# Kernel tuning notes

Hardware: AMD Instinct MI355X
Metric: run time of the kernel (lower is better)

Reference implementation:

```python
import jax, jax.numpy as jnp
import numpy as np

B, D, H = 4096, 1024, 1024  # batch, input_size, hidden_size


def setup_inputs() -> dict:
    key = jax.random.key(0)
    ks = jax.random.split(key, 7)
    stdv = 1.0 / np.sqrt(H)
    u = lambda k, shape: jax.random.uniform(k, shape, jnp.float32, -stdv, stdv)
    return {
        "x": jax.random.normal(ks[0], (B, D), jnp.float32),
        "h0": jax.random.normal(ks[1], (1, B, H), jnp.float32),
        "c0": jax.random.normal(ks[2], (1, B, H), jnp.float32),
        "w_ih": u(ks[3], (4 * H, D)),
        "w_hh": u(ks[4], (4 * H, H)),
        "b_ih": u(ks[5], (4 * H,)),
        "b_hh": u(ks[6], (4 * H,)),
    }


def lstm_cell(x, h, c, w_ih, w_hh, b_ih, b_hh):
    # gates: [B, 4H] = x @ w_ih^T + b_ih + h @ w_hh^T + b_hh
    gates = x @ w_ih.T + h @ w_hh.T + (b_ih + b_hh)
    i, f, g, o = jnp.split(gates, 4, axis=1)
    c_new = jax.nn.sigmoid(f) * c + jax.nn.sigmoid(i) * jnp.tanh(g)
    h_new = jax.nn.sigmoid(o) * jnp.tanh(c_new)
    return h_new, c_new


def reference(x, h0, c0, w_ih, w_hh, b_ih, b_hh):
    # num_layers = 1 (the only well-formed config of the original module)
    h, c = lstm_cell(x, h0[0], c0[0], w_ih, w_hh, b_ih, b_hh)
    return h, c
```

## Files before the change

kernel.cpp:

```cpp
#include <hip/hip_runtime.h>
#include <hip/hip_bf16.h>

#define TB 4096
#define TD 1024
#define TH 1024
#define TK 2048
#define KSTEPS 32

typedef _Float16 f16;
typedef _Float16 f16x8 __attribute__((ext_vector_type(8)));
typedef _Float16 f16x4 __attribute__((ext_vector_type(4)));
typedef float f32x4 __attribute__((ext_vector_type(4)));

__device__ __forceinline__ void gload16(const void* g, void* l) {
  __builtin_amdgcn_global_load_lds(
      (const __attribute__((address_space(1))) void*)g,
      (__attribute__((address_space(3))) void*)l, 16, 0, 0);
}

__global__ void __launch_bounds__(256) k_convert(
    const float* __restrict__ x, const float* __restrict__ h0,
    const float* __restrict__ w_ih, const float* __restrict__ w_hh,
    f16* __restrict__ Uh, f16* __restrict__ Wh) {
  int t = blockIdx.x * 256 + threadIdx.x;
  const int perMat = (TB * TK) / 4;
  const bool isW = t >= perMat;
  int tt = isW ? t - perMat : t;
  size_t e0 = (size_t)tt * 4;
  int row = (int)(e0 >> 11);
  int k = (int)(e0 & (TK - 1));
  const float* src;
  if (!isW)
    src = (k < TD) ? (x + (size_t)row * TD + k) : (h0 + (size_t)row * TH + (k - TD));
  else
    src = (k < TD) ? (w_ih + (size_t)row * TD + k) : (w_hh + (size_t)row * TH + (k - TD));
  float4 v = *(const float4*)src;
  f16x4 o;
  o[0] = (f16)v.x; o[1] = (f16)v.y; o[2] = (f16)v.z; o[3] = (f16)v.w;
  *(f16x4*)((isW ? Wh : Uh) + e0) = o;
}

__global__ void __launch_bounds__(256) k_lstm(
    const f16* __restrict__ Uh, const f16* __restrict__ Wh,
    const float* __restrict__ b_ih, const float* __restrict__ b_hh,
    const float* __restrict__ c0, float* __restrict__ h_out,
    float* __restrict__ c_out) {
  __shared__ char lds[32768];
  const int tid = threadIdx.x;
  const int l = tid & 63;
  const int w = tid >> 6;

  int bid = blockIdx.x;
  int swz = (bid & 7) * 128 + (bid >> 3);
  const int bm = swz >> 5;
  const int bn = swz & 31;
  const int rowBase = bm * 128;
  const int hcBase = bn * 32;

  const int srow = l >> 3;
  const int g = (l & 7) ^ srow;
  size_t aoff[4], boff[4];
#pragma unroll
  for (int j = 0; j < 4; ++j) {
    int rt = w * 32 + j * 8 + srow;
    aoff[j] = (size_t)(rowBase + rt) * TK + g * 8;
    int wr = ((rt >> 5) << 10) + hcBase + (rt & 31);
    boff[j] = (size_t)wr * TK + g * 8;
  }

  const int fr = l & 15;
  const int fq = l >> 4;
  const int s0 = ((fq ^ (fr & 7)) << 4);
  const int s1 = (((4 + fq) ^ (fr & 7)) << 4);
  const int aRow = (w * 32 + fr) * 128;

  f32x4 acc[2][8] = {};

  for (int kt = 0; kt < KSTEPS; ++kt) {
    const size_t k0 = (size_t)kt * 64;
#pragma unroll
    for (int j = 0; j < 4; ++j)
      gload16(Uh + aoff[j] + k0, lds + w * 4096 + j * 1024);
#pragma unroll
    for (int j = 0; j < 4; ++j)
      gload16(Wh + boff[j] + k0, lds + 16384 + w * 4096 + j * 1024);
    __syncthreads();

    f16x8 a[2][2];
#pragma unroll
    for (int m = 0; m < 2; ++m) {
      a[m][0] = *(const f16x8*)(lds + aRow + m * 2048 + s0);
      a[m][1] = *(const f16x8*)(lds + aRow + m * 2048 + s1);
    }
#pragma unroll
    for (int n = 0; n < 8; ++n) {
      const int bRow = 16384 + (n * 16 + fr) * 128;
      f16x8 b0 = *(const f16x8*)(lds + bRow + s0);
      f16x8 b1 = *(const f16x8*)(lds + bRow + s1);
      acc[0][n] = __builtin_amdgcn_mfma_f32_16x16x32_f16(a[0][0], b0, acc[0][n], 0, 0, 0);
      acc[1][n] = __builtin_amdgcn_mfma_f32_16x16x32_f16(a[1][0], b0, acc[1][n], 0, 0, 0);
      acc[0][n] = __builtin_amdgcn_mfma_f32_16x16x32_f16(a[0][1], b1, acc[0][n], 0, 0, 0);
      acc[1][n] = __builtin_amdgcn_mfma_f32_16x16x32_f16(a[1][1], b1, acc[1][n], 0, 0, 0);
    }
    __syncthreads();
  }

  const int cl = l & 15;
  const int rsub = fq * 4;
#pragma unroll
  for (int n0 = 0; n0 < 2; ++n0) {
    const int hc = hcBase + n0 * 16 + cl;
    const float bi = b_ih[hc] + b_hh[hc];
    const float bfv = b_ih[TH + hc] + b_hh[TH + hc];
    const float bg = b_ih[2 * TH + hc] + b_hh[2 * TH + hc];
    const float bo = b_ih[3 * TH + hc] + b_hh[3 * TH + hc];
#pragma unroll
    for (int m = 0; m < 2; ++m) {
#pragma unroll
      for (int r = 0; r < 4; ++r) {
        const int row = rowBase + w * 32 + m * 16 + rsub + r;
        float gi = acc[m][n0 + 0][r] + bi;
        float gf = acc[m][n0 + 2][r] + bfv;
        float gg = acc[m][n0 + 4][r] + bg;
        float go = acc[m][n0 + 6][r] + bo;
        float cprev = c0[(size_t)row * TH + hc];
        float ig = 1.0f / (1.0f + __expf(-gi));
        float fg = 1.0f / (1.0f + __expf(-gf));
        float og = 1.0f / (1.0f + __expf(-go));
        float cn = fg * cprev + ig * tanhf(gg);
        float hn = og * tanhf(cn);
        h_out[(size_t)row * TH + hc] = hn;
        c_out[(size_t)row * TH + hc] = cn;
      }
    }
  }
}

extern "C" void kernel_launch(void* const* d_in, const int* in_sizes, int n_in,
                              void* d_out, int out_size, void* d_ws, size_t ws_size,
                              hipStream_t stream) {
  const float* x    = (const float*)d_in[0];
  const float* h0   = (const float*)d_in[1];
  const float* c0   = (const float*)d_in[2];
  const float* w_ih = (const float*)d_in[3];
  const float* w_hh = (const float*)d_in[4];
  const float* b_ih = (const float*)d_in[5];
  const float* b_hh = (const float*)d_in[6];

  float* h_out = (float*)d_out;
  float* c_out = h_out + (size_t)TB * TH;

  f16* Uh = (f16*)d_ws;
  f16* Wh = Uh + (size_t)TB * TK;

  const int convBlocks = (2 * TB * TK / 4) / 256;
  k_convert<<<convBlocks, 256, 0, stream>>>(x, h0, w_ih, w_hh, Uh, Wh);
  k_lstm<<<1024, 256, 0, stream>>>(Uh, Wh, b_ih, b_hh, c0, h_out, c_out);
}
```

Baseline: 239.9 us.

## Enlarge GEMM tile to 256x256 with triple-buffered LDS pipeline

Moves the fused LSTM GEMM to 512-thread blocks with 256 rows by 64 hidden columns (256 gate columns), each wave computing a 128x64 sub-tile. It adds a three-stage LDS ring buffer with K-step 32, prefetches two steps ahead, and uses one barrier per step with explicit vmcnt waits, so global-to-LDS loads overlap MFMA work. The aim is more data reuse per LDS byte and hidden load latency. The cost is 96KB of dynamic LDS, more accumulator registers, and only 256 blocks for the GPU's CUs.

```diff
diff --git a/kernel.cpp b/kernel.cpp
--- a/kernel.cpp
+++ b/kernel.cpp
@@ -5,14 +5,16 @@
 #define TD 1024
 #define TH 1024
 #define TK 2048
-#define KSTEPS 32
+#define NT 64
+#define BUF_SZ 32768
+#define B_OFF 16384
 
 typedef _Float16 f16;
 typedef _Float16 f16x8 __attribute__((ext_vector_type(8)));
 typedef _Float16 f16x4 __attribute__((ext_vector_type(4)));
 typedef float f32x4 __attribute__((ext_vector_type(4)));
 
-__device__ __forceinline__ void gload16(const void* g, void* l) {
+__device__ __forceinline__ void gload16(const f16* g, const char* l) {
   __builtin_amdgcn_global_load_lds(
       (const __attribute__((address_space(1))) void*)g,
       (__attribute__((address_space(3))) void*)l, 16, 0, 0);
@@ -40,98 +42,110 @@
   *(f16x4*)((isW ? Wh : Uh) + e0) = o;
 }
 
-__global__ void __launch_bounds__(256) k_lstm(
+__global__ void __launch_bounds__(512, 2) k_lstm(
     const f16* __restrict__ Uh, const f16* __restrict__ Wh,
     const float* __restrict__ b_ih, const float* __restrict__ b_hh,
     const float* __restrict__ c0, float* __restrict__ h_out,
     float* __restrict__ c_out) {
-  __shared__ char lds[32768];
+  extern __shared__ char lds[];
   const int tid = threadIdx.x;
   const int l = tid & 63;
   const int w = tid >> 6;
+  const int wm = w >> 2;
+  const int wc = w & 3;
 
   int bid = blockIdx.x;
-  int swz = (bid & 7) * 128 + (bid >> 3);
-  const int bm = swz >> 5;
-  const int bn = swz & 31;
-  const int rowBase = bm * 128;
-  const int hcBase = bn * 32;
+  int swz = (bid & 7) * 32 + (bid >> 3);
+  const int bm = swz >> 4;
+  const int bn = swz & 15;
+  const int rowBase = bm * 256;
+  const int hcBase = bn * 64;
 
-  const int srow = l >> 3;
-  const int g = (l & 7) ^ srow;
-  size_t aoff[4], boff[4];
-#pragma unroll
-  for (int j = 0; j < 4; ++j) {
-    int rt = w * 32 + j * 8 + srow;
-    aoff[j] = (size_t)(rowBase + rt) * TK + g * 8;
-    int wr = ((rt >> 5) << 10) + hcBase + (rt & 31);
-    boff[j] = (size_t)wr * TK + g * 8;
-  }
+  const int g = (l & 3) ^ ((l >> 3) & 3);
+  const int rl = l >> 2;
+  const int cA0 = w, cA1 = 8 + w;
+  const f16* aP0 = Uh + (size_t)(rowBase + cA0 * 16 + rl) * TK + g * 8;
+  const f16* aP1 = Uh + (size_t)(rowBase + cA1 * 16 + rl) * TK + g * 8;
+  const f16* bP0 = Wh + (size_t)((cA0 & 3) * 1024 + hcBase + rl + (cA0 >> 2) * 16) * TK + g * 8;
+  const f16* bP1 = Wh + (size_t)((cA1 & 3) * 1024 + hcBase + rl + (cA1 >> 2) * 16) * TK + g * 8;
 
   const int fr = l & 15;
   const int fq = l >> 4;
-  const int s0 = ((fq ^ (fr & 7)) << 4);
-  const int s1 = (((4 + fq) ^ (fr & 7)) << 4);
-  const int aRow = (w * 32 + fr) * 128;
+  const int slot = ((fq ^ ((fr >> 1) & 3)) << 4);
+  const int aAddr = (wm * 128 + fr) * 64 + slot;
+  const int bAddr = B_OFF + (wc * 64 + fr) * 64 + slot;
 
-  f32x4 acc[2][8] = {};
+  f32x4 acc[8][4] = {};
 
-  for (int kt = 0; kt < KSTEPS; ++kt) {
-    const size_t k0 = (size_t)kt * 64;
+  gload16(aP0, lds + 0 * BUF_SZ + cA0 * 1024);
+  gload16(aP1, lds + 0 * BUF_SZ + cA1 * 1024);
+  gload16(bP0, lds + 0 * BUF_SZ + B_OFF + cA0 * 1024);
+  gload16(bP1, lds + 0 * BUF_SZ + B_OFF + cA1 * 1024);
+  gload16(aP0 + 32, lds + 1 * BUF_SZ + cA0 * 1024);
+  gload16(aP1 + 32, lds + 1 * BUF_SZ + cA1 * 1024);
+  gload16(bP0 + 32, lds + 1 * BUF_SZ + B_OFF + cA0 * 1024);
+  gload16(bP1 + 32, lds + 1 * BUF_SZ + B_OFF + cA1 * 1024);
+  asm volatile("s_waitcnt vmcnt(4)" ::: "memory");
+  __builtin_amdgcn_sched_barrier(0);
+  __builtin_amdgcn_s_barrier();
+
+  int offR = 0;
+  int offS = 2 * BUF_SZ;
+  for (int t = 0; t < NT; ++t) {
+    if (t < NT - 2) {
+      const int ke = (t + 2) * 32;
+      gload16(aP0 + ke, lds + offS + cA0 * 1024);
+      gload16(aP1 + ke, lds + offS + cA1 * 1024);
+      gload16(bP0 + ke, lds + offS + B_OFF + cA0 * 1024);
+      gload16(bP1 + ke, lds + offS + B_OFF + cA1 * 1024);
+    }
+    const char* baseA = lds + offR + aAddr;
+    const char* baseB = lds + offR + bAddr;
+    f16x8 af[8], bf[4];
 #pragma unroll
-    for (int j = 0; j < 4; ++j)
-      gload16(Uh + aoff[j] + k0, lds + w * 4096 + j * 1024);
+    for (int m = 0; m < 8; ++m) af[m] = *(const f16x8*)(baseA + m * 1024);
 #pragma unroll
-    for (int j = 0; j < 4; ++j)
-      gload16(Wh + boff[j] + k0, lds + 16384 + w * 4096 + j * 1024);
-    __syncthreads();
-
-    f16x8 a[2][2];
+    for (int n = 0; n < 4; ++n) bf[n] = *(const f16x8*)(baseB + n * 1024);
+    __builtin_amdgcn_s_setprio(1);
 #pragma unroll
-    for (int m = 0; m < 2; ++m) {
-      a[m][0] = *(const f16x8*)(lds + aRow + m * 2048 + s0);
-      a[m][1] = *(const f16x8*)(lds + aRow + m * 2048 + s1);
-    }
+    for (int m = 0; m < 8; ++m)
 #pragma unroll
-    for (int n = 0; n < 8; ++n) {
-      const int bRow = 16384 + (n * 16 + fr) * 128;
-      f16x8 b0 = *(const f16x8*)(lds + bRow + s0);
-      f16x8 b1 = *(const f16x8*)(lds + bRow + s1);
-      acc[0][n] = __builtin_amdgcn_mfma_f32_16x16x32_f16(a[0][0], b0, acc[0][n], 0, 0, 0);
-      acc[1][n] = __builtin_amdgcn_mfma_f32_16x16x32_f16(a[1][0], b0, acc[1][n], 0, 0, 0);
-      acc[0][n] = __builtin_amdgcn_mfma_f32_16x16x32_f16(a[0][1], b1, acc[0][n], 0, 0, 0);
-      acc[1][n] = __builtin_amdgcn_mfma_f32_16x16x32_f16(a[1][1], b1, acc[1][n], 0, 0, 0);
-    }
-    __syncthreads();
+      for (int n = 0; n < 4; ++n)
+        acc[m][n] = __builtin_amdgcn_mfma_f32_16x16x32_f16(af[m], bf[n], acc[m][n], 0, 0, 0);
+    __builtin_amdgcn_s_setprio(0);
+    asm volatile("s_waitcnt lgkmcnt(0)" ::: "memory");
+    if (t < NT - 2)
+      asm volatile("s_waitcnt vmcnt(4)" ::: "memory");
+    else
+      asm volatile("s_waitcnt vmcnt(0)" ::: "memory");
+    __builtin_amdgcn_sched_barrier(0);
+    __builtin_amdgcn_s_barrier();
+    offR = (offR == 2 * BUF_SZ) ? 0 : offR + BUF_SZ;
+    offS = (offS == 2 * BUF_SZ) ? 0 : offS + BUF_SZ;
   }
 
-  const int cl = l & 15;
-  const int rsub = fq * 4;
+  const int hc = hcBase + wc * 16 + fr;
+  const float bi = b_ih[hc] + b_hh[hc];
+  const float bfv = b_ih[TH + hc] + b_hh[TH + hc];
+  const float bg = b_ih[2 * TH + hc] + b_hh[2 * TH + hc];
+  const float bo = b_ih[3 * TH + hc] + b_hh[3 * TH + hc];
 #pragma unroll
-  for (int n0 = 0; n0 < 2; ++n0) {
-    const int hc = hcBase + n0 * 16 + cl;
-    const float bi = b_ih[hc] + b_hh[hc];
-    const float bfv = b_ih[TH + hc] + b_hh[TH + hc];
-    const float bg = b_ih[2 * TH + hc] + b_hh[2 * TH + hc];
-    const float bo = b_ih[3 * TH + hc] + b_hh[3 * TH + hc];
+  for (int m = 0; m < 8; ++m) {
 #pragma unroll
-    for (int m = 0; m < 2; ++m) {
-#pragma unroll
-      for (int r = 0; r < 4; ++r) {
-        const int row = rowBase + w * 32 + m * 16 + rsub + r;
-        float gi = acc[m][n0 + 0][r] + bi;
-        float gf = acc[m][n0 + 2][r] + bfv;
-        float gg = acc[m][n0 + 4][r] + bg;
-        float go = acc[m][n0 + 6][r] + bo;
-        float cprev = c0[(size_t)row * TH + hc];
-        float ig = 1.0f / (1.0f + __expf(-gi));
-        float fg = 1.0f / (1.0f + __expf(-gf));
-        float og = 1.0f / (1.0f + __expf(-go));
-        float cn = fg * cprev + ig * tanhf(gg);
-        float hn = og * tanhf(cn);
-        h_out[(size_t)row * TH + hc] = hn;
-        c_out[(size_t)row * TH + hc] = cn;
-      }
+    for (int r = 0; r < 4; ++r) {
+      const int row = rowBase + wm * 128 + m * 16 + fq * 4 + r;
+      float gi = acc[m][0][r] + bi;
+      float gf = acc[m][1][r] + bfv;
+      float gg = acc[m][2][r] + bg;
+      float go = acc[m][3][r] + bo;
+      float cprev = c0[(size_t)row * TH + hc];
+      float ig = 1.0f / (1.0f + __expf(-gi));
+      float fg = 1.0f / (1.0f + __expf(-gf));
+      float og = 1.0f / (1.0f + __expf(-go));
+      float cn = fg * cprev + ig * tanhf(gg);
+      float hn = og * tanhf(cn);
+      h_out[(size_t)row * TH + hc] = hn;
+      c_out[(size_t)row * TH + hc] = cn;
     }
   }
 }
@@ -155,5 +169,9 @@
 
   const int convBlocks = (2 * TB * TK / 4) / 256;
   k_convert<<<convBlocks, 256, 0, stream>>>(x, h0, w_ih, w_hh, Uh, Wh);
-  k_lstm<<<1024, 256, 0, stream>>>(Uh, Wh, b_ih, b_hh, c0, h_out, c_out);
+
+  static_assert(3 * BUF_SZ == 98304, "lds");
+  (void)hipFuncSetAttribute((const void*)k_lstm,
+                            hipFuncAttributeMaxDynamicSharedMemorySize, 3 * BUF_SZ);
+  k_lstm<<<256, 512, 3 * BUF_SZ, stream>>>(Uh, Wh, b_ih, b_hh, c0, h_out, c_out);
 }
```

Result: faster. 211.5 us (-11.8%).
